# Optimization experiments

Hardware: AMD Instinct MI355X
Metric: run time of the kernel (lower is better)

## Reference

```python
import jax, jax.numpy as jnp
import numpy as np

H = 1024   # hidden_size
NH = 16    # num heads
HD = H // NH


def setup_inputs() -> dict:
    key = jax.random.key(0)
    ks = jax.random.split(key, 6)
    B, S = 4, 2048
    hidden_states = jax.random.normal(ks[0], (B, S, H), dtype=jnp.float32)
    attention_mask = jnp.zeros((B, S), dtype=jnp.float32)  # additive mask
    scale = 1.0 / np.sqrt(H)
    Wq = jax.random.normal(ks[1], (H, H), dtype=jnp.float32) * scale
    Wk = jax.random.normal(ks[2], (H, H), dtype=jnp.float32) * scale
    Wv = jax.random.normal(ks[3], (H, H), dtype=jnp.float32) * scale
    Wo = jax.random.normal(ks[4], (H, H), dtype=jnp.float32) * scale
    return {"hidden_states": hidden_states, "attention_mask": attention_mask,
            "Wq": Wq, "Wk": Wk, "Wv": Wv, "Wo": Wo}


def reference(hidden_states, attention_mask, Wq, Wk, Wv, Wo):
    B, S, _ = hidden_states.shape
    scaling = HD ** -0.5
    # nn.Linear: y = x @ W.T ; split heads -> [B, NH, S, HD]
    def heads(x, W):
        return (x @ W.T).reshape(B, S, NH, HD).transpose(0, 2, 1, 3)
    q = heads(hidden_states, Wq)
    k = heads(hidden_states, Wk)
    v = heads(hidden_states, Wv)
    scores = jnp.einsum('bhqd,bhkd->bhqk', q, k) * scaling
    scores = scores + attention_mask[:, None, None, :]
    weights = jax.nn.softmax(scores, axis=-1)
    attn = jnp.einsum('bhqk,bhkd->bhqd', weights, v)
    attn = attn.transpose(0, 2, 1, 3).reshape(B, S, H)
    return attn @ Wo.T
```

## Files before the change

kernel.cpp:

```cpp
#include <hip/hip_runtime.h>
#include <hip/hip_bf16.h>

#define B_ 4
#define S_ 2048
#define H_ 1024
#define NH_ 16
#define HD_ 64
#define QSCALE 0.1803368801111204f

typedef __bf16 bf16_t;
typedef bf16_t bf16x8 __attribute__((ext_vector_type(8)));
typedef bf16_t bf16x4 __attribute__((ext_vector_type(4)));
typedef bf16_t bf16x2t __attribute__((ext_vector_type(2)));
typedef float f32x4 __attribute__((ext_vector_type(4)));
typedef unsigned u32x2 __attribute__((ext_vector_type(2)));
typedef unsigned u32x4 __attribute__((ext_vector_type(4)));

__device__ __forceinline__ f32x4 mfma16(bf16x8 a, bf16x8 b, f32x4 c) {
  return __builtin_amdgcn_mfma_f32_16x16x32_bf16(a, b, c, 0, 0, 0);
}

extern "C" __device__ float __ocml_native_exp2_f32(float);
__device__ __forceinline__ float fast_exp2(float x) {
  return __ocml_native_exp2_f32(x);
}

__device__ __forceinline__ void gll16(const bf16_t* g, bf16_t* l) {
  __builtin_amdgcn_global_load_lds(
      (const __attribute__((address_space(1))) void*)g,
      (__attribute__((address_space(3))) void*)l, 16, 0, 0);
}

__device__ __forceinline__ bf16x8 frag64(const bf16_t* lds, int row,
                                         int kchunk) {
  return *(const bf16x8*)((const char*)lds + row * 128 +
                          ((kchunk ^ (row & 7)) << 4));
}

__device__ __forceinline__ void stage128(const bf16_t* gbase, int gstride,
                                         bf16_t* lds, int w, int lane) {
#pragma unroll
  for (int j = 0; j < 4; ++j) {
    int seg = w * 4 + j;
    int row = seg * 8 + (lane >> 3);
    int chunk = (lane & 7) ^ (row & 7);
    gll16(gbase + (size_t)row * gstride + chunk * 8, lds + seg * 512);
  }
}

__global__ __launch_bounds__(256) void cvt_all(
    const float* __restrict__ X, const float* __restrict__ Wq,
    const float* __restrict__ Wk, const float* __restrict__ Wv,
    const float* __restrict__ Wo, const float* __restrict__ mask,
    bf16_t* __restrict__ Xb, bf16_t* __restrict__ Wqb,
    bf16_t* __restrict__ Wkb, bf16_t* __restrict__ Wvb,
    bf16_t* __restrict__ Wob, float* __restrict__ maskl) {
  size_t i = ((size_t)blockIdx.x * 256 + threadIdx.x) * 4;
  const float* src;
  bf16_t* dst;
  size_t off;
  float scale = 1.0f;
  if (i < 8388608) {
    src = X; dst = Xb; off = i;
  } else {
    size_t j = i - 8388608;
    if (j >= 4194304) {
      size_t mo = j - 4194304;
      float4 mv = *(const float4*)(mask + mo);
      const float LOG2E = 1.4426950408889634f;
      float4 ml = {mv.x * LOG2E, mv.y * LOG2E, mv.z * LOG2E, mv.w * LOG2E};
      *(float4*)(maskl + mo) = ml;
      return;
    }
    int w = (int)(j >> 20);
    off = j & 1048575;
    switch (w) {
      case 0: src = Wq; dst = Wqb; scale = QSCALE; break;
      case 1: src = Wk; dst = Wkb; break;
      case 2: src = Wv; dst = Wvb; break;
      default: src = Wo; dst = Wob; break;
    }
  }
  float4 v = *(const float4*)(src + off);
  bf16x4 o = {(bf16_t)(v.x * scale), (bf16_t)(v.y * scale),
              (bf16_t)(v.z * scale), (bf16_t)(v.w * scale)};
  *(bf16x4*)(dst + off) = o;
}

__device__ __forceinline__ void gemm_core(const bf16_t* __restrict__ A,
                                          const bf16_t* __restrict__ Bw,
                                          int Mb, int Nb, bf16_t* As,
                                          bf16_t* Bs, f32x4 (*acc)[4], int w,
                                          int lane, int quad, int l15, int wm,
                                          int wn) {
  for (int kb = 0; kb < 16; ++kb) {
    stage128(A + (size_t)Mb * 1024 + kb * 64, 1024, As, w, lane);
    stage128(Bw + (size_t)Nb * 1024 + kb * 64, 1024, Bs, w, lane);
    __syncthreads();
#pragma unroll
    for (int kt = 0; kt < 2; ++kt) {
      bf16x8 af[4], bfr[4];
#pragma unroll
      for (int i = 0; i < 4; ++i) {
        af[i] = frag64(As, wm * 64 + i * 16 + l15, kt * 4 + quad);
        bfr[i] = frag64(Bs, wn * 64 + i * 16 + l15, kt * 4 + quad);
      }
      __builtin_amdgcn_s_setprio(1);
#pragma unroll
      for (int mt = 0; mt < 4; ++mt)
#pragma unroll
        for (int nt = 0; nt < 4; ++nt)
          acc[mt][nt] = mfma16(af[mt], bfr[nt], acc[mt][nt]);
      __builtin_amdgcn_s_setprio(0);
    }
    __syncthreads();
  }
}

__global__ __launch_bounds__(256) void gemm_qkv(
    const bf16_t* __restrict__ Xb, const bf16_t* __restrict__ Wqb,
    const bf16_t* __restrict__ Wkb, const bf16_t* __restrict__ Wvb,
    bf16_t* __restrict__ q_ws, bf16_t* __restrict__ k_ws,
    bf16_t* __restrict__ vt_ws) {
  __shared__ __align__(16) bf16_t As[8192];
  __shared__ __align__(16) bf16_t Bs[8192];
  int w = threadIdx.x >> 6, lane = threadIdx.x & 63;
  int quad = lane >> 4, l15 = lane & 15;
  int wm = w >> 1, wn = w & 1;
  int z = blockIdx.z;
  const bf16_t* A = (z == 2) ? Wvb : Xb;
  const bf16_t* Bw = (z == 0) ? Wqb : ((z == 1) ? Wkb : Xb);
  int Mb = (z == 2) ? blockIdx.y * 128 : blockIdx.x * 128;
  int Nb = (z == 2) ? blockIdx.x * 128 : blockIdx.y * 128;
  f32x4 acc[4][4] = {};
  gemm_core(A, Bw, Mb, Nb, As, Bs, acc, w, lane, quad, l15, wm, wn);
  if (z != 2) {
    bf16_t* O = (z == 0) ? q_ws : k_ws;
#pragma unroll
    for (int mt = 0; mt < 4; ++mt) {
      int m0t = Mb + wm * 64 + mt * 16;
#pragma unroll
      for (int nt = 0; nt < 4; ++nt) {
        int n0t = Nb + wn * 64 + nt * 16;
        int h = n0t >> 6, d = (n0t & 63) + l15;
#pragma unroll
        for (int r = 0; r < 4; ++r) {
          int tok = m0t + quad * 4 + r;
          int b = tok >> 11, s = tok & 2047;
          O[(((size_t)b * NH_ + h) * S_ + s) * HD_ + d] = (bf16_t)acc[mt][nt][r];
        }
      }
    }
  } else {
#pragma unroll
    for (int mt = 0; mt < 4; ++mt) {
      int m0t = Mb + wm * 64 + mt * 16;
#pragma unroll
      for (int nt = 0; nt < 4; ++nt) {
        int n0t = Nb + wn * 64 + nt * 16;
#pragma unroll
        for (int r = 0; r < 4; ++r) {
          int dg = m0t + quad * 4 + r;
          int hh = dg >> 6, d = dg & 63;
          int tok = n0t + l15;
          int b = tok >> 11, s = tok & 2047;
          vt_ws[((size_t)(b * NH_ + hh) * HD_ + d) * S_ + s] =
              (bf16_t)acc[mt][nt][r];
        }
      }
    }
  }
}

__global__ __launch_bounds__(256) void gemm_out(
    const bf16_t* __restrict__ A, const bf16_t* __restrict__ Bw,
    float* __restrict__ out) {
  __shared__ __align__(16) bf16_t As[8192];
  __shared__ __align__(16) bf16_t Bs[8192];
  int w = threadIdx.x >> 6, lane = threadIdx.x & 63;
  int quad = lane >> 4, l15 = lane & 15;
  int wm = w >> 1, wn = w & 1;
  int Mb = blockIdx.x * 128, Nb = blockIdx.y * 128;
  f32x4 acc[4][4] = {};
  gemm_core(A, Bw, Mb, Nb, As, Bs, acc, w, lane, quad, l15, wm, wn);
#pragma unroll
  for (int mt = 0; mt < 4; ++mt) {
    int m0t = Mb + wm * 64 + mt * 16;
#pragma unroll
    for (int nt = 0; nt < 4; ++nt) {
      int n0t = Nb + wn * 64 + nt * 16;
#pragma unroll
      for (int r = 0; r < 4; ++r)
        out[(size_t)(m0t + quad * 4 + r) * 1024 + n0t + l15] = acc[mt][nt][r];
    }
  }
}

__global__ __launch_bounds__(256, 3) void attn_fused(
    const bf16_t* __restrict__ Q, const bf16_t* __restrict__ K,
    const bf16_t* __restrict__ Vt, const float* __restrict__ maskl,
    bf16_t* __restrict__ Oa) {
  __shared__ __align__(16) bf16_t Ks[2][4096];
  __shared__ __align__(16) bf16_t Vs[2][4096];
  int w = threadIdx.x >> 6, lane = threadIdx.x & 63;
  int quad = lane >> 4, l15 = lane & 15;
  int bh = blockIdx.y;
  int b = bh >> 4, h = bh & 15;
  int q0 = blockIdx.x * 128 + w * 32;
  const bf16_t* Qh = Q + (size_t)bh * (S_ * HD_);
  const bf16_t* Kh = K + (size_t)bh * (S_ * HD_);
  const bf16_t* Vh = Vt + (size_t)bh * (HD_ * S_);
  const float* mb = maskl + b * S_;
  const bf16_t one_b = (bf16_t)1.0f;
  bf16x8 ones = {one_b, one_b, one_b, one_b, one_b, one_b, one_b, one_b};

  int srow[2], schunk[2], lseg[2];
#pragma unroll
  for (int j = 0; j < 2; ++j) {
    int seg = w * 2 + j;
    srow[j] = seg * 8 + (lane >> 3);
    schunk[j] = (lane & 7) ^ (srow[j] & 7);
    lseg[j] = seg * 512;
  }

  bf16x8 qf[2][2];
#pragma unroll
  for (int nt = 0; nt < 2; ++nt)
#pragma unroll
    for (int kt = 0; kt < 2; ++kt)
      qf[nt][kt] = *(const bf16x8*)(Qh + (size_t)(q0 + nt * 16 + l15) * HD_ +
                                    kt * 32 + quad * 8);

  f32x4 oc[4][2] = {};
  f32x4 lc[2] = {};

#pragma unroll
  for (int j = 0; j < 2; ++j) {
    gll16(Kh + (size_t)srow[j] * HD_ + schunk[j] * 8, &Ks[0][0] + lseg[j]);
    gll16(Vh + (size_t)srow[j] * S_ + schunk[j] * 8, &Vs[0][0] + lseg[j]);
  }
  f32x4 mreg[4];
#pragma unroll
  for (int mt = 0; mt < 4; ++mt)
    mreg[mt] = *(const f32x4*)(mb + mt * 16 + quad * 4);
  __syncthreads();

  for (int c = 0; c < 32; ++c) {
    int cur = c & 1;
    if (c + 1 < 32) {
      const bf16_t* Kc = Kh + (size_t)(c + 1) * 64 * HD_;
      const bf16_t* Vc = Vh + (size_t)(c + 1) * 64;
#pragma unroll
      for (int j = 0; j < 2; ++j) {
        gll16(Kc + (size_t)srow[j] * HD_ + schunk[j] * 8,
              &Ks[cur ^ 1][0] + lseg[j]);
        gll16(Vc + (size_t)srow[j] * S_ + schunk[j] * 8,
              &Vs[cur ^ 1][0] + lseg[j]);
      }
    }
    f32x4 mcur[4];
#pragma unroll
    for (int mt = 0; mt < 4; ++mt) mcur[mt] = mreg[mt];
    if (c + 1 < 32) {
#pragma unroll
      for (int mt = 0; mt < 4; ++mt)
        mreg[mt] = *(const f32x4*)(mb + (c + 1) * 64 + mt * 16 + quad * 4);
    }
    f32x4 sc[4][2] = {};
#pragma unroll
    for (int kt = 0; kt < 2; ++kt) {
      bf16x8 kf[4];
#pragma unroll
      for (int mt = 0; mt < 4; ++mt)
        kf[mt] = frag64(Ks[cur], mt * 16 + l15, kt * 4 + quad);
#pragma unroll
      for (int mt = 0; mt < 4; ++mt)
#pragma unroll
        for (int nt = 0; nt < 2; ++nt)
          sc[mt][nt] = mfma16(kf[mt], qf[nt][kt], sc[mt][nt]);
    }
#pragma unroll
    for (int kt = 0; kt < 2; ++kt) {
      unsigned pk[2][2][2];
#pragma unroll
      for (int mi = 0; mi < 2; ++mi) {
        int mt = kt * 2 + mi;
#pragma unroll
        for (int nt = 0; nt < 2; ++nt) {
          f32x4 e = sc[mt][nt] + mcur[mt];
          f32x4 p;
#pragma unroll
          for (int r = 0; r < 4; ++r) p[r] = fast_exp2(e[r]);
          bf16x2t h0 = {(bf16_t)p[0], (bf16_t)p[1]};
          bf16x2t h1 = {(bf16_t)p[2], (bf16_t)p[3]};
          pk[mi][nt][0] = __builtin_bit_cast(unsigned, h0);
          pk[mi][nt][1] = __builtin_bit_cast(unsigned, h1);
        }
      }
      bf16x8 pf[2];
#pragma unroll
      for (int nt = 0; nt < 2; ++nt) {
        u32x2 a0 = __builtin_amdgcn_permlane32_swap(pk[0][nt][0],
                                                    pk[1][nt][0],
                                                    false, false);
        u32x2 b0 = __builtin_amdgcn_permlane16_swap(a0.x, a0.y, false, false);
        u32x2 a1 = __builtin_amdgcn_permlane32_swap(pk[0][nt][1],
                                                    pk[1][nt][1],
                                                    false, false);
        u32x2 b1 = __builtin_amdgcn_permlane16_swap(a1.x, a1.y, false, false);
        u32x4 pu = {b0.x, b1.x, b0.y, b1.y};
        pf[nt] = __builtin_bit_cast(bf16x8, pu);
      }
      lc[0] = mfma16(ones, pf[0], lc[0]);
      lc[1] = mfma16(ones, pf[1], lc[1]);
#pragma unroll
      for (int dt = 0; dt < 4; ++dt) {
        bf16x8 vf = frag64(Vs[cur], dt * 16 + l15, kt * 4 + quad);
#pragma unroll
        for (int nt = 0; nt < 2; ++nt)
          oc[dt][nt] = mfma16(vf, pf[nt], oc[dt][nt]);
      }
    }
    __syncthreads();
  }
  float inv[2] = {1.0f / lc[0][0], 1.0f / lc[1][0]};
#pragma unroll
  for (int dt = 0; dt < 4; ++dt)
#pragma unroll
    for (int nt = 0; nt < 2; ++nt) {
      bf16x4 o4;
#pragma unroll
      for (int r = 0; r < 4; ++r) o4[r] = (bf16_t)(oc[dt][nt][r] * inv[nt]);
      size_t tok = (size_t)b * S_ + q0 + nt * 16 + l15;
      *(bf16x4*)(Oa + tok * H_ + h * HD_ + dt * 16 + quad * 4) = o4;
    }
}

extern "C" void kernel_launch(void* const* d_in, const int* in_sizes, int n_in,
                              void* d_out, int out_size, void* d_ws,
                              size_t ws_size, hipStream_t stream) {
  const float* hs   = (const float*)d_in[0];
  const float* mask = (const float*)d_in[1];
  const float* Wq   = (const float*)d_in[2];
  const float* Wk   = (const float*)d_in[3];
  const float* Wv   = (const float*)d_in[4];
  const float* Wo   = (const float*)d_in[5];
  float* out = (float*)d_out;

  char* p = (char*)d_ws;
  bf16_t* Xb  = (bf16_t*)p; p += (size_t)8192 * 1024 * 2;
  bf16_t* Wqb = (bf16_t*)p; p += (size_t)1024 * 1024 * 2;
  bf16_t* Wkb = (bf16_t*)p; p += (size_t)1024 * 1024 * 2;
  bf16_t* Wvb = (bf16_t*)p; p += (size_t)1024 * 1024 * 2;
  bf16_t* Wob = (bf16_t*)p; p += (size_t)1024 * 1024 * 2;
  bf16_t* q_ws  = (bf16_t*)p; p += (size_t)8192 * 1024 * 2;
  bf16_t* k_ws  = (bf16_t*)p; p += (size_t)8192 * 1024 * 2;
  bf16_t* vt_ws = (bf16_t*)p; p += (size_t)8192 * 1024 * 2;
  float* maskl = (float*)p; p += (size_t)B_ * S_ * 4;
  bf16_t* attn_b = Xb;

  cvt_all<<<12296, 256, 0, stream>>>(hs, Wq, Wk, Wv, Wo, mask, Xb, Wqb, Wkb,
                                     Wvb, Wob, maskl);
  gemm_qkv<<<dim3(64, 8, 3), 256, 0, stream>>>(Xb, Wqb, Wkb, Wvb, q_ws, k_ws,
                                               vt_ws);
  attn_fused<<<dim3(16, 64), 256, 0, stream>>>(q_ws, k_ws, vt_ws, maskl,
                                               attn_b);
  gemm_out<<<dim3(64, 8), 256, 0, stream>>>(attn_b, Wob, out);
}
```

Before: 270.8 us.

## Use 512-thread attention blocks with head-major grid and mask-initialized accumulators

The attention kernel now runs 8 waves per block covering 256 queries, so each staged K/V tile is shared by twice as many queries. Each thread loads one chunk instead of two, and the grid is reordered so blocks of the same head are adjacent. The score accumulators start from the mask values, which removes a separate add before the exponential. The larger block raises register pressure and lowers the occupancy target to 2 blocks per CU.

```diff
diff --git a/kernel.cpp b/kernel.cpp
--- a/kernel.cpp
+++ b/kernel.cpp
@@ -196,7 +196,7 @@
   }
 }
 
-__global__ __launch_bounds__(256, 3) void attn_fused(
+__global__ __launch_bounds__(512, 2) void attn_fused(
     const bf16_t* __restrict__ Q, const bf16_t* __restrict__ K,
     const bf16_t* __restrict__ Vt, const float* __restrict__ maskl,
     bf16_t* __restrict__ Oa) {
@@ -204,9 +204,9 @@
   __shared__ __align__(16) bf16_t Vs[2][4096];
   int w = threadIdx.x >> 6, lane = threadIdx.x & 63;
   int quad = lane >> 4, l15 = lane & 15;
-  int bh = blockIdx.y;
+  int bh = blockIdx.x;
   int b = bh >> 4, h = bh & 15;
-  int q0 = blockIdx.x * 128 + w * 32;
+  int q0 = blockIdx.y * 256 + w * 32;
   const bf16_t* Qh = Q + (size_t)bh * (S_ * HD_);
   const bf16_t* Kh = K + (size_t)bh * (S_ * HD_);
   const bf16_t* Vh = Vt + (size_t)bh * (HD_ * S_);
@@ -214,14 +214,9 @@
   const bf16_t one_b = (bf16_t)1.0f;
   bf16x8 ones = {one_b, one_b, one_b, one_b, one_b, one_b, one_b, one_b};
 
-  int srow[2], schunk[2], lseg[2];
-#pragma unroll
-  for (int j = 0; j < 2; ++j) {
-    int seg = w * 2 + j;
-    srow[j] = seg * 8 + (lane >> 3);
-    schunk[j] = (lane & 7) ^ (srow[j] & 7);
-    lseg[j] = seg * 512;
-  }
+  int srow = w * 8 + (lane >> 3);
+  int schunk = (lane & 7) ^ (srow & 7);
+  int lseg = w * 512;
 
   bf16x8 qf[2][2];
 #pragma unroll
@@ -234,11 +229,8 @@
   f32x4 oc[4][2] = {};
   f32x4 lc[2] = {};
 
-#pragma unroll
-  for (int j = 0; j < 2; ++j) {
-    gll16(Kh + (size_t)srow[j] * HD_ + schunk[j] * 8, &Ks[0][0] + lseg[j]);
-    gll16(Vh + (size_t)srow[j] * S_ + schunk[j] * 8, &Vs[0][0] + lseg[j]);
-  }
+  gll16(Kh + (size_t)srow * HD_ + schunk * 8, &Ks[0][0] + lseg);
+  gll16(Vh + (size_t)srow * S_ + schunk * 8, &Vs[0][0] + lseg);
   f32x4 mreg[4];
 #pragma unroll
   for (int mt = 0; mt < 4; ++mt)
@@ -249,24 +241,20 @@
     int cur = c & 1;
     if (c + 1 < 32) {
       const bf16_t* Kc = Kh + (size_t)(c + 1) * 64 * HD_;
-      const bf16_t* Vc = Vh + (size_t)(c + 1) * 64;
-#pragma unroll
-      for (int j = 0; j < 2; ++j) {
-        gll16(Kc + (size_t)srow[j] * HD_ + schunk[j] * 8,
-              &Ks[cur ^ 1][0] + lseg[j]);
-        gll16(Vc + (size_t)srow[j] * S_ + schunk[j] * 8,
-              &Vs[cur ^ 1][0] + lseg[j]);
-      }
-    }
-    f32x4 mcur[4];
-#pragma unroll
-    for (int mt = 0; mt < 4; ++mt) mcur[mt] = mreg[mt];
+      const bf16_t* Vc = Vt == nullptr ? nullptr : Vh + (size_t)(c + 1) * 64;
+      gll16(Kc + (size_t)srow * HD_ + schunk * 8, &Ks[cur ^ 1][0] + lseg);
+      gll16(Vc + (size_t)srow * S_ + schunk * 8, &Vs[cur ^ 1][0] + lseg);
+    }
+    f32x4 sc[4][2];
+#pragma unroll
+    for (int mt = 0; mt < 4; ++mt)
+#pragma unroll
+      for (int nt = 0; nt < 2; ++nt) sc[mt][nt] = mreg[mt];
     if (c + 1 < 32) {
 #pragma unroll
       for (int mt = 0; mt < 4; ++mt)
         mreg[mt] = *(const f32x4*)(mb + (c + 1) * 64 + mt * 16 + quad * 4);
     }
-    f32x4 sc[4][2] = {};
 #pragma unroll
     for (int kt = 0; kt < 2; ++kt) {
       bf16x8 kf[4];
@@ -287,10 +275,9 @@
         int mt = kt * 2 + mi;
 #pragma unroll
         for (int nt = 0; nt < 2; ++nt) {
-          f32x4 e = sc[mt][nt] + mcur[mt];
           f32x4 p;
 #pragma unroll
-          for (int r = 0; r < 4; ++r) p[r] = fast_exp2(e[r]);
+          for (int r = 0; r < 4; ++r) p[r] = fast_exp2(sc[mt][nt][r]);
           bf16x2t h0 = {(bf16_t)p[0], (bf16_t)p[1]};
           bf16x2t h1 = {(bf16_t)p[2], (bf16_t)p[3]};
           pk[mi][nt][0] = __builtin_bit_cast(unsigned, h0);
@@ -363,7 +350,7 @@
                                      Wvb, Wob, maskl);
   gemm_qkv<<<dim3(64, 8, 3), 256, 0, stream>>>(Xb, Wqb, Wkb, Wvb, q_ws, k_ws,
                                                vt_ws);
-  attn_fused<<<dim3(16, 64), 256, 0, stream>>>(q_ws, k_ws, vt_ws, maskl,
-                                               attn_b);
+  attn_fused<<<dim3(64, 8), 512, 0, stream>>>(q_ws, k_ws, vt_ws, maskl,
+                                              attn_b);
   gemm_out<<<dim3(64, 8), 256, 0, stream>>>(attn_b, Wob, out);
 }
```

Result: faster. 250.1 us (median of 2 runs) (-7.6%).
